# Performance work log

Hardware: AMD Instinct MI355X
Metric: run time of the kernel (lower is better)

The kernel has to match this reference:

```python
import jax, jax.numpy as jnp
import numpy as np


def setup_inputs() -> dict:
    key = jax.random.key(0)
    k1, k2, k3, k4 = jax.random.split(key, 4)
    B, D, N, M = 4, 256, 4096, 4096
    return {
        "src": jax.random.normal(k1, (B, 3, N), dtype=jnp.float32),
        "tgt": jax.random.normal(k2, (B, 3, M), dtype=jnp.float32),
        "src_emb": jax.random.normal(k3, (B, D, N), dtype=jnp.float32),
        "tgt_emb": jax.random.normal(k4, (B, D, M), dtype=jnp.float32),
    }


def reference(src, tgt, src_emb, tgt_emb):
    # pairwise_distance[b,n,m] = -||src_emb[:,n] - tgt_emb[:,m]||^2
    # decomposed as -xx + 2*inner - yy (inner below is -2*dot, as in torch code)
    inner = -2.0 * jnp.einsum("bdn,bdm->bnm", src_emb, tgt_emb)       # [B,N,M]
    xx = jnp.sum(src_emb ** 2, axis=1)[:, :, None]                     # [B,N,1]
    yy = jnp.sum(tgt_emb ** 2, axis=1)[:, None, :]                     # [B,1,M]
    pairwise_distance = -xx - inner - yy                               # [B,N,M]
    scores = jax.nn.softmax(pairwise_distance, axis=2)                 # softmax over tgt points
    # src_corr[b,c,n] = sum_m tgt[b,c,m] * scores[b,n,m]
    src_corr = jnp.einsum("bcm,bnm->bcn", tgt, scores)                 # [B,3,N]
    return src_corr
```

## Files before the change

### kernel.cpp

```cpp
#include <hip/hip_runtime.h>

#define NBATCH 4
#define DDIM   256
#define NN     4096
#define MM     4096
#define NCHUNK 8
#define MCHUNK 512
#define MTILE  64
#define PAIRB  1040
#define SUBB   (32 * PAIRB)
#define LOG2E  1.44269504088896340736f

using half8   = __attribute__((ext_vector_type(8))) _Float16;
using floatx4 = __attribute__((ext_vector_type(4))) float;

__global__ __launch_bounds__(256) void k_prep(const float* __restrict__ src_emb,
                                              const float* __restrict__ tgt_emb,
                                              const float* __restrict__ tgt,
                                              _Float16* __restrict__ Qh,
                                              _Float16* __restrict__ Kh,
                                              float* __restrict__ yyS,
                                              float4* __restrict__ Vt) {
    __shared__ float psum[4][64];
    int i = blockIdx.x;
    int xcd = i & 7, j = i >> 3;
    int b = xcd >> 1, nhalf = xcd & 1;
    int tensor = j & 1, sub = j >> 1;
    int n0 = nhalf * 2048 + sub * 64;
    const float* in = tensor ? tgt_emb : src_emb;
    _Float16* outp  = tensor ? Kh : Qh;
    const float scale = tensor ? 1.0f : 2.0f * LOG2E;
    int t = threadIdx.x, w = t >> 6, ln = t & 63;
    const float* ib = in + (size_t)b * DDIM * NN + n0 + ln;
    _Float16* op = outp + (size_t)(b * NN + n0 + ln) * DDIM;
    float ss = 0.f;
#pragma unroll
    for (int itr = 0; itr < 8; itr++) {
        int dg = w + itr * 4;
        half8 h;
#pragma unroll
        for (int k = 0; k < 8; k++) {
            float f = ib[(size_t)(dg * 8 + k) * NN];
            ss = fmaf(f, f, ss);
            h[k] = (_Float16)(f * scale);
        }
        *(half8*)(op + dg * 8) = h;
    }
    if (tensor) psum[w][ln] = ss;
    __syncthreads();
    if (tensor) {
        if (t < 64) {
            float s = psum[0][t] + psum[1][t] + psum[2][t] + psum[3][t];
            yyS[b * MM + n0 + t] = s * (-LOG2E);
        } else if (t < 128) {
            int m = n0 + (t - 64);
            const float* tp = tgt + (size_t)b * 3 * MM + m;
            Vt[(size_t)b * MM + m] = make_float4(tp[0], tp[MM], tp[2 * MM], 1.0f);
        }
    }
}

__global__ __launch_bounds__(256, 2) void k_flash(const _Float16* __restrict__ Qh,
                                                  const _Float16* __restrict__ Kh,
                                                  const float* __restrict__ yyS,
                                                  const float4* __restrict__ Vt,
                                                  float4* __restrict__ Opart,
                                                  float* __restrict__ Mpart) {
    __shared__ __align__(16) char Kt[2 * SUBB];
    __shared__ floatx4 vtt[MCHUNK];
    __shared__ floatx4 yyt[MCHUNK / 4];

    int i = blockIdx.x, t = threadIdx.x;
    int xcd = i & 7, j = i >> 3;
    int b = xcd >> 1, nhalf = xcd & 1;
    int chunk = j & 7, ntile = nhalf * 8 + (j >> 3);

    int wave = t >> 6, lane = t & 63, quad = lane >> 4, l15 = lane & 15;
    int n0 = ntile * 256 + wave * 64;
    int m0 = chunk * MCHUNK;

    const _Float16* kp = Kh + (size_t)b * MM * DDIM;
    int dg = lane & 31, rh = lane >> 5;
    auto stage = [&](int mt) {
        const _Float16* gb = kp + (size_t)(m0 + mt * MTILE) * DDIM;
        char* lb = &Kt[(mt & 1) * SUBB];
#pragma unroll
        for (int it = 0; it < 8; it++) {
            int pr = wave * 8 + it;
            __builtin_amdgcn_global_load_lds(
                (const __attribute__((address_space(1))) uint32_t*)(const void*)
                    (gb + (size_t)(pr * 2 + rh) * DDIM + dg * 8),
                (__attribute__((address_space(3))) uint32_t*)(void*)
                    (lb + pr * PAIRB),
                16, 0, 0);
        }
    };

    stage(0);

    {
        const float4* vb = Vt + (size_t)b * MM + m0;
        for (int r = t; r < MCHUNK; r += 256) {
            float4 g = vb[r];
            vtt[r] = (floatx4){g.x, g.y, g.z, g.w};
        }
        const floatx4* yb = (const floatx4*)(yyS + (size_t)b * MM + m0);
        if (t < MCHUNK / 4) yyt[t] = yb[t];
    }

    const _Float16* qp = Qh + (size_t)b * NN * DDIM;
    half8 qf[4][8];
#pragma unroll
    for (int nb = 0; nb < 4; nb++) {
        int n = n0 + nb * 16 + l15;
#pragma unroll
        for (int ds = 0; ds < 8; ds++)
            qf[nb][ds] = *(const half8*)(qp + (size_t)n * DDIM + (ds * 4 + quad) * 8);
    }

    const floatx4 z4 = {0.f, 0.f, 0.f, 0.f};
    floatx4 o[4] = {z4, z4, z4, z4};
    float mr[4];
#pragma unroll
    for (int nb = 0; nb < 4; nb++) mr[nb] = -__builtin_inff();

    for (int mt = 0; mt < MCHUNK / MTILE; mt++) {
        __syncthreads();
        if (mt + 1 < MCHUNK / MTILE) stage(mt + 1);

        const char* Kb = &Kt[(mt & 1) * SUBB];
#pragma unroll
        for (int mb = 0; mb < 4; mb++) {
            half8 a[8];
            {
                int rho = mb * 16 + l15;
                const char* rb = Kb + (rho >> 1) * PAIRB + (rho & 1) * 512 + quad * 16;
#pragma unroll
                for (int ds = 0; ds < 8; ds++) a[ds] = *(const half8*)(rb + ds * 64);
            }
            floatx4 acc[4] = {z4, z4, z4, z4};
#pragma unroll
            for (int ds = 0; ds < 8; ds++)
#pragma unroll
                for (int nb = 0; nb < 4; nb++)
                    acc[nb] = __builtin_amdgcn_mfma_f32_16x16x32_f16(a[ds], qf[nb][ds], acc[nb], 0, 0, 0);

            floatx4 yv = yyt[mt * 16 + mb * 4 + quad];
            floatx4 vr[4];
#pragma unroll
            for (int r = 0; r < 4; r++) vr[r] = vtt[mt * MTILE + mb * 16 + quad * 4 + r];
#pragma unroll
            for (int nb = 0; nb < 4; nb++) {
                acc[nb] = acc[nb] + yv;
                float tm = fmaxf(fmaxf(acc[nb][0], acc[nb][1]), fmaxf(acc[nb][2], acc[nb][3]));
                float mn = fmaxf(mr[nb], tm);
                float al = __builtin_amdgcn_exp2f(mr[nb] - mn);
                mr[nb] = mn;
                o[nb] = o[nb] * al;
#pragma unroll
                for (int r = 0; r < 4; r++) {
                    float p = __builtin_amdgcn_exp2f(acc[nb][r] - mn);
                    o[nb] = o[nb] + p * vr[r];
                }
            }
        }
    }

#pragma unroll
    for (int nb = 0; nb < 4; nb++) {
        float mq = mr[nb];
        float ma = fmaxf(mq, __shfl_xor(mq, 16, 64));
        ma = fmaxf(ma, __shfl_xor(ma, 32, 64));
        float wgt = __builtin_amdgcn_exp2f(mq - ma);
        floatx4 ow = o[nb] * wgt;
#pragma unroll
        for (int c = 0; c < 4; c++) {
            float v = ow[c];
            v += __shfl_xor(v, 16, 64);
            v += __shfl_xor(v, 32, 64);
            ow[c] = v;
        }
        if (quad == 0) {
            int n = n0 + nb * 16 + l15;
            size_t idx = (size_t)(chunk * NBATCH + b) * NN + n;
            Opart[idx] = make_float4(ow[0], ow[1], ow[2], ow[3]);
            Mpart[idx] = ma;
        }
    }
}

__global__ __launch_bounds__(128) void k_combine(const float4* __restrict__ Opart,
                                                 const float* __restrict__ Mpart,
                                                 float* __restrict__ out) {
    int idx = blockIdx.x * 128 + threadIdx.x;
    int b = idx >> 12, n = idx & (NN - 1);
    float mstar = -__builtin_inff();
#pragma unroll
    for (int j = 0; j < NCHUNK; j++)
        mstar = fmaxf(mstar, Mpart[(size_t)(j * NBATCH + b) * NN + n]);
    float o0 = 0.f, o1 = 0.f, o2 = 0.f, l = 0.f;
#pragma unroll
    for (int j = 0; j < NCHUNK; j++) {
        size_t id = (size_t)(j * NBATCH + b) * NN + n;
        float w = __builtin_amdgcn_exp2f(Mpart[id] - mstar);
        float4 P = Opart[id];
        o0 = fmaf(w, P.x, o0); o1 = fmaf(w, P.y, o1);
        o2 = fmaf(w, P.z, o2); l  = fmaf(w, P.w, l);
    }
    out[(size_t)(b * 3 + 0) * NN + n] = o0 / l;
    out[(size_t)(b * 3 + 1) * NN + n] = o1 / l;
    out[(size_t)(b * 3 + 2) * NN + n] = o2 / l;
}

extern "C" void kernel_launch(void* const* d_in, const int* in_sizes, int n_in,
                              void* d_out, int out_size, void* d_ws, size_t ws_size,
                              hipStream_t stream) {
    const float* tgt     = (const float*)d_in[1];
    const float* src_emb = (const float*)d_in[2];
    const float* tgt_emb = (const float*)d_in[3];
    float* out = (float*)d_out;

    char* ws = (char*)d_ws;
    _Float16* Qh  = (_Float16*)(ws);
    _Float16* Kh  = (_Float16*)(ws + 8388608);
    float*    yyS = (float*)   (ws + 16777216);
    float4*   Vt  = (float4*)  (ws + 16842752);
    float4*   Op  = (float4*)  (ws + 17104896);
    float*    Mp  = (float*)   (ws + 19202048);

    hipLaunchKernelGGL(k_prep,    dim3(512), dim3(256), 0, stream,
                       src_emb, tgt_emb, tgt, Qh, Kh, yyS, Vt);
    hipLaunchKernelGGL(k_flash,   dim3(512), dim3(256), 0, stream, Qh, Kh, yyS, Vt, Op, Mp);
    hipLaunchKernelGGL(k_combine, dim3(128), dim3(128), 0, stream, Op, Mp, out);
}
```

Baseline: 133.4 us.

## Store Q/K fp16 in MFMA fragment-ordered layout for contiguous loads

The prep kernel now writes the fp16 Q and K tensors in a blocked layout ordered like the MFMA fragments (16-row blocks, by ds, then quad, then lane). The flash kernel can then stage K tiles into LDS with fully contiguous 16-byte-per-lane copies and read A fragments at lane*16 strides, with no padded pair layout. Q fragment loads become coalesced too. The intent is to remove LDS bank conflicts and scattered global accesses. The catch is that the prep kernel's writes are more scattered and the LDS read pattern loses its padding.

After: 125.9 us (median of 2 runs). 5.7% less time.

```diff
diff --git a/kernel.cpp b/kernel.cpp
--- a/kernel.cpp
+++ b/kernel.cpp
@@ -7,18 +7,17 @@
 #define NCHUNK 8
 #define MCHUNK 512
 #define MTILE  64
-#define PAIRB  1040
-#define SUBB   (32 * PAIRB)
 #define LOG2E  1.44269504088896340736f
 
 using half8   = __attribute__((ext_vector_type(8))) _Float16;
 using floatx4 = __attribute__((ext_vector_type(4))) float;
+
 
 __global__ __launch_bounds__(256) void k_prep(const float* __restrict__ src_emb,
                                               const float* __restrict__ tgt_emb,
                                               const float* __restrict__ tgt,
-                                              _Float16* __restrict__ Qh,
-                                              _Float16* __restrict__ Kh,
+                                              _Float16* __restrict__ Qf,
+                                              _Float16* __restrict__ Kf,
                                               float* __restrict__ yyS,
                                               float4* __restrict__ Vt) {
     __shared__ float psum[4][64];
@@ -28,23 +27,27 @@
     int tensor = j & 1, sub = j >> 1;
     int n0 = nhalf * 2048 + sub * 64;
     const float* in = tensor ? tgt_emb : src_emb;
-    _Float16* outp  = tensor ? Kh : Qh;
+    _Float16* outp  = tensor ? Kf : Qf;
     const float scale = tensor ? 1.0f : 2.0f * LOG2E;
     int t = threadIdx.x, w = t >> 6, ln = t & 63;
     const float* ib = in + (size_t)b * DDIM * NN + n0 + ln;
-    _Float16* op = outp + (size_t)(b * NN + n0 + ln) * DDIM;
+    _Float16* ob = outp + (size_t)b * NN * 32 * 8;
+    int blk = (n0 + ln) >> 4, l15 = ln & 15;
     float ss = 0.f;
 #pragma unroll
-    for (int itr = 0; itr < 8; itr++) {
-        int dg = w + itr * 4;
-        half8 h;
-#pragma unroll
-        for (int k = 0; k < 8; k++) {
-            float f = ib[(size_t)(dg * 8 + k) * NN];
-            ss = fmaf(f, f, ss);
-            h[k] = (_Float16)(f * scale);
-        }
-        *(half8*)(op + dg * 8) = h;
+    for (int h = 0; h < 2; h++) {
+        int ds = w + h * 4;
+#pragma unroll
+        for (int oct = 0; oct < 4; oct++) {
+            half8 v;
+#pragma unroll
+            for (int k = 0; k < 8; k++) {
+                float f = ib[(size_t)(ds * 32 + oct * 8 + k) * NN];
+                ss = fmaf(f, f, ss);
+                v[k] = (_Float16)(f * scale);
+            }
+            *(half8*)(ob + ((((size_t)blk * 8 + ds) * 4 + oct) * 16 + l15) * 8) = v;
+        }
     }
     if (tensor) psum[w][ln] = ss;
     __syncthreads();
@@ -60,13 +63,13 @@
     }
 }
 
-__global__ __launch_bounds__(256, 2) void k_flash(const _Float16* __restrict__ Qh,
-                                                  const _Float16* __restrict__ Kh,
+__global__ __launch_bounds__(256, 2) void k_flash(const _Float16* __restrict__ Qf,
+                                                  const _Float16* __restrict__ Kf,
                                                   const float* __restrict__ yyS,
                                                   const float4* __restrict__ Vt,
                                                   float4* __restrict__ Opart,
                                                   float* __restrict__ Mpart) {
-    __shared__ __align__(16) char Kt[2 * SUBB];
+    __shared__ __align__(16) _Float16 Kt[2][MTILE * DDIM];
     __shared__ floatx4 vtt[MCHUNK];
     __shared__ floatx4 yyt[MCHUNK / 4];
 
@@ -76,22 +79,20 @@
     int chunk = j & 7, ntile = nhalf * 8 + (j >> 3);
 
     int wave = t >> 6, lane = t & 63, quad = lane >> 4, l15 = lane & 15;
-    int n0 = ntile * 256 + wave * 64;
     int m0 = chunk * MCHUNK;
-
-    const _Float16* kp = Kh + (size_t)b * MM * DDIM;
-    int dg = lane & 31, rh = lane >> 5;
+    int mblk0 = m0 >> 4;
+
+    const char* kfb = (const char*)(Kf + (size_t)b * NN * DDIM);
     auto stage = [&](int mt) {
-        const _Float16* gb = kp + (size_t)(m0 + mt * MTILE) * DDIM;
-        char* lb = &Kt[(mt & 1) * SUBB];
+        const char* gb = kfb + (size_t)(mblk0 + mt * 4) * 8192 + wave * 8192;
+        char* lb = (char*)&Kt[mt & 1][0] + wave * 8192;
 #pragma unroll
         for (int it = 0; it < 8; it++) {
-            int pr = wave * 8 + it;
             __builtin_amdgcn_global_load_lds(
                 (const __attribute__((address_space(1))) uint32_t*)(const void*)
-                    (gb + (size_t)(pr * 2 + rh) * DDIM + dg * 8),
+                    (gb + it * 1024 + lane * 16),
                 (__attribute__((address_space(3))) uint32_t*)(void*)
-                    (lb + pr * PAIRB),
+                    (lb + it * 1024),
                 16, 0, 0);
         }
     };
@@ -108,15 +109,14 @@
         if (t < MCHUNK / 4) yyt[t] = yb[t];
     }
 
-    const _Float16* qp = Qh + (size_t)b * NN * DDIM;
+    int nblk0 = ntile * 16 + wave * 4;
+    const half8* qp = (const half8*)Qf + (size_t)b * NN * 32;
     half8 qf[4][8];
 #pragma unroll
-    for (int nb = 0; nb < 4; nb++) {
-        int n = n0 + nb * 16 + l15;
+    for (int nb = 0; nb < 4; nb++)
 #pragma unroll
         for (int ds = 0; ds < 8; ds++)
-            qf[nb][ds] = *(const half8*)(qp + (size_t)n * DDIM + (ds * 4 + quad) * 8);
-    }
+            qf[nb][ds] = qp[(((size_t)(nblk0 + nb) * 8 + ds) * 4 + quad) * 16 + l15];
 
     const floatx4 z4 = {0.f, 0.f, 0.f, 0.f};
     floatx4 o[4] = {z4, z4, z4, z4};
@@ -128,16 +128,14 @@
         __syncthreads();
         if (mt + 1 < MCHUNK / MTILE) stage(mt + 1);
 
-        const char* Kb = &Kt[(mt & 1) * SUBB];
+        const char* Kb = (const char*)&Kt[mt & 1][0];
 #pragma unroll
         for (int mb = 0; mb < 4; mb++) {
+            const char* rb = Kb + mb * 8192 + lane * 16;
             half8 a[8];
-            {
-                int rho = mb * 16 + l15;
-                const char* rb = Kb + (rho >> 1) * PAIRB + (rho & 1) * 512 + quad * 16;
-#pragma unroll
-                for (int ds = 0; ds < 8; ds++) a[ds] = *(const half8*)(rb + ds * 64);
-            }
+#pragma unroll
+            for (int ds = 0; ds < 8; ds++) a[ds] = *(const half8*)(rb + ds * 1024);
+
             floatx4 acc[4] = {z4, z4, z4, z4};
 #pragma unroll
             for (int ds = 0; ds < 8; ds++)
@@ -181,7 +179,7 @@
             ow[c] = v;
         }
         if (quad == 0) {
-            int n = n0 + nb * 16 + l15;
+            int n = (nblk0 + nb) * 16 + l15;
             size_t idx = (size_t)(chunk * NBATCH + b) * NN + n;
             Opart[idx] = make_float4(ow[0], ow[1], ow[2], ow[3]);
             Mpart[idx] = ma;
@@ -221,15 +219,15 @@
     float* out = (float*)d_out;
 
     char* ws = (char*)d_ws;
-    _Float16* Qh  = (_Float16*)(ws);
-    _Float16* Kh  = (_Float16*)(ws + 8388608);
+    _Float16* Qf  = (_Float16*)(ws);
+    _Float16* Kf  = (_Float16*)(ws + 8388608);
     float*    yyS = (float*)   (ws + 16777216);
     float4*   Vt  = (float4*)  (ws + 16842752);
     float4*   Op  = (float4*)  (ws + 17104896);
     float*    Mp  = (float*)   (ws + 19202048);
 
     hipLaunchKernelGGL(k_prep,    dim3(512), dim3(256), 0, stream,
-                       src_emb, tgt_emb, tgt, Qh, Kh, yyS, Vt);
-    hipLaunchKernelGGL(k_flash,   dim3(512), dim3(256), 0, stream, Qh, Kh, yyS, Vt, Op, Mp);
+                       src_emb, tgt_emb, tgt, Qf, Kf, yyS, Vt);
+    hipLaunchKernelGGL(k_flash,   dim3(512), dim3(256), 0, stream, Qf, Kf, yyS, Vt, Op, Mp);
     hipLaunchKernelGGL(k_combine, dim3(128), dim3(128), 0, stream, Op, Mp, out);
 }
```
